# Performance work log

Hardware: AMD Instinct MI355X
Metric: run time of the kernel (lower is better)

The kernel has to match this reference:

```python
import jax, jax.numpy as jnp
import numpy as np

DIM = 128      # token feature dim
HEADS = 4
HEAD_DIM = DIM // HEADS
H = 512
W = 512
NSP = 4096     # n_spixels = H*W/scale
TEMP = DIM ** (-0.5)   # NOTE: original scales by full-dim ** -0.5
NEG = -9.0e15
EPS = 1e-12    # torch F.normalize eps


def setup_inputs() -> dict:
    key = jax.random.key(0)
    k1, k2, k3, k4 = jax.random.split(key, 4)
    return {
        "spf": jax.random.normal(k1, (DIM, NSP), jnp.float32),
        "segments": jax.random.randint(k2, (H, W), 0, NSP, jnp.int32),
        "w_qkv": jax.random.normal(k3, (DIM, 3 * DIM), jnp.float32) / np.sqrt(DIM),
        "w_out": jax.random.normal(k4, (DIM, DIM), jnp.float32) / np.sqrt(DIM),
        "b_out": jnp.zeros((DIM,), jnp.float32),
    }


def build_adjacency(seg, n_sp):
    """Vectorized version of get_A: for every 2x2 window (i in [0,h-3], j in [0,w-3])
    connect the max and min superpixel labels; zero the diagonal."""
    a = seg[:-2, :-2]
    b = seg[:-2, 1:-1]
    c = seg[1:-1, :-2]
    d = seg[1:-1, 1:-1]
    mx = jnp.maximum(jnp.maximum(a, b), jnp.maximum(c, d)).ravel()
    mn = jnp.minimum(jnp.minimum(a, b), jnp.minimum(c, d)).ravel()
    A = jnp.zeros((n_sp, n_sp), jnp.float32)
    A = A.at[mx, mn].set(1.0)
    A = A.at[mn, mx].set(1.0)
    # fill_diagonal(A, 0) (also removes windows where max == min)
    A = A * (1.0 - jnp.eye(n_sp, dtype=jnp.float32))
    return A


def _l2norm(t):
    n = jnp.sqrt(jnp.sum(t * t, axis=-1, keepdims=True))
    return t / jnp.maximum(n, EPS)


def reference(spf, segments, w_qkv, w_out, b_out):
    A = build_adjacency(segments, NSP)                      # [n, n]
    x = spf.T                                               # [n, dim]
    qkv = x @ w_qkv                                         # [n, 3*dim]
    q, k, v = jnp.split(qkv, 3, axis=-1)
    split = lambda t: t.reshape(NSP, HEADS, HEAD_DIM).transpose(1, 0, 2)  # [h, n, d]
    q, k, v = split(q), split(k), split(v)
    q = _l2norm(q)
    k = _l2norm(k)
    # Original masks per-head scores, then keeps only head 0's attention
    # (attn[0][0]) and broadcasts it over all heads' v. We compute only
    # head 0's scores (mathematically identical output).
    scores = (q[0] @ k[0].T) * TEMP                         # [n, n] cosine scores
    scores = jnp.where(A > 0, scores, NEG)
    eye = jnp.eye(NSP, dtype=bool)
    scores = jnp.where(eye, 1.0, scores)                    # np.fill_diagonal(attn, 1)
    attn = jax.nn.softmax(scores, axis=-1)                  # [n, n]
    out = jnp.einsum('nm,hmd->hnd', attn, v)                # shared attn over heads
    out = out.transpose(1, 0, 2).reshape(NSP, DIM)          # [n, dim]
    out = out @ w_out + b_out                               # to_out Linear
    # map_sp2p: scatter superpixel features back to pixel grid (hard assignment)
    pix = out[segments]                                     # [H, W, dim]
    return pix.transpose(2, 0, 1)[None]                     # [1, dim, H, W]
```

## Files before the change

### kernel.cpp

```cpp
#include <hip/hip_runtime.h>

#define NSP 4096
#define HW 512
#define TEMP 0.08838834764831845f
#define MAXE 768

__global__ void zero_mask(unsigned int* __restrict__ mask) {
    int i = blockIdx.x * blockDim.x + threadIdx.x;
    ((uint4*)mask)[i] = make_uint4(0u, 0u, 0u, 0u);
}

__global__ void build_adj(const int* __restrict__ seg, unsigned int* __restrict__ mask) {
    int idx = blockIdx.x * blockDim.x + threadIdx.x;
    const int NW = 510 * 510;
    if (idx >= NW) return;
    int i = idx / 510, j = idx - i * 510;
    const int* r = seg + i * HW + j;
    int a = r[0], b = r[1], c = r[HW], d = r[HW + 1];
    int mx = max(max(a, b), max(c, d));
    int mn = min(min(a, b), min(c, d));
    if (mx == mn) return;
    atomicOr(&mask[mx * 128 + (mn >> 5)], 1u << (mn & 31));
    atomicOr(&mask[mn * 128 + (mx >> 5)], 1u << (mx & 31));
}

__global__ void qkv_gemm(const float* __restrict__ spf, const float* __restrict__ wqkv,
                         float* __restrict__ Q0, float* __restrict__ K0,
                         float* __restrict__ V) {
    int gid = blockIdx.x * blockDim.x + threadIdx.x;
    int g = gid % 48;
    int n = gid / 48;
    int wcol;
    float* outp;
    if (g < 8)       { wcol = g * 4;              outp = Q0 + n * 32  + g * 4; }
    else if (g < 16) { wcol = 128 + (g - 8) * 4;  outp = K0 + n * 32  + (g - 8) * 4; }
    else             { wcol = 256 + (g - 16) * 4; outp = V  + n * 128 + (g - 16) * 4; }
    float4 acc = {0.f, 0.f, 0.f, 0.f};
#pragma unroll 8
    for (int d = 0; d < 128; ++d) {
        float x = spf[d * NSP + n];
        float4 w = *(const float4*)(wqkv + d * 384 + wcol);
        acc.x += x * w.x; acc.y += x * w.y; acc.z += x * w.z; acc.w += x * w.w;
    }
    *(float4*)outp = acc;
}

__global__ void l2norm_qk(float* __restrict__ Q0, float* __restrict__ K0) {
    int t = blockIdx.x * blockDim.x + threadIdx.x;
    float* p = (t < NSP) ? (Q0 + t * 32) : (K0 + (t - NSP) * 32);
    float4* p4 = (float4*)p;
    float4 v[8];
    float s = 0.f;
#pragma unroll
    for (int i = 0; i < 8; ++i) {
        v[i] = p4[i];
        s += v[i].x * v[i].x + v[i].y * v[i].y + v[i].z * v[i].z + v[i].w * v[i].w;
    }
    float inv = 1.0f / fmaxf(sqrtf(s), 1e-12f);
#pragma unroll
    for (int i = 0; i < 8; ++i) {
        v[i].x *= inv; v[i].y *= inv; v[i].z *= inv; v[i].w *= inv;
        p4[i] = v[i];
    }
}

__global__ void __launch_bounds__(128) sparse_attn(
    const unsigned int* __restrict__ mask, const float* __restrict__ Q0,
    const float* __restrict__ K0, const float* __restrict__ V,
    float* __restrict__ out) {
    int n = blockIdx.x;
    int t = threadIdx.x;
    __shared__ int   midx[MAXE];
    __shared__ float wts[MAXE];
    __shared__ int   cnt;
    __shared__ float q0s[32];
    if (t == 0) cnt = 0;
    if (t < 32) q0s[t] = Q0[n * 32 + t];
    __syncthreads();

    unsigned int w = mask[n * 128 + t];
    while (w) {
        int b = __ffs(w) - 1;
        w &= w - 1;
        int m = t * 32 + b;
        const float4* kp = (const float4*)(K0 + m * 32);
        float s = 0.f;
#pragma unroll
        for (int i = 0; i < 8; ++i) {
            float4 kv = kp[i];
            s += q0s[i * 4 + 0] * kv.x + q0s[i * 4 + 1] * kv.y +
                 q0s[i * 4 + 2] * kv.z + q0s[i * 4 + 3] * kv.w;
        }
        float wt = __expf(s * TEMP - 1.0f);
        int pos = atomicAdd(&cnt, 1);
        if (pos < MAXE) { midx[pos] = m; wts[pos] = wt; }
    }
    __syncthreads();

    int c = min(cnt, MAXE);
    float acc  = V[n * 128 + t];
    float wsum = 1.0f;
    int e = 0;
    for (; e + 4 <= c; e += 4) {
        float w0 = wts[e],  w1 = wts[e + 1], w2 = wts[e + 2], w3 = wts[e + 3];
        int   m0 = midx[e], m1 = midx[e + 1], m2 = midx[e + 2], m3 = midx[e + 3];
        float v0 = V[m0 * 128 + t];
        float v1 = V[m1 * 128 + t];
        float v2 = V[m2 * 128 + t];
        float v3 = V[m3 * 128 + t];
        acc  += w0 * v0 + w1 * v1 + w2 * v2 + w3 * v3;
        wsum += w0 + w1 + w2 + w3;
    }
    for (; e < c; ++e) {
        float wt = wts[e];
        acc  += wt * V[midx[e] * 128 + t];
        wsum += wt;
    }
    out[n * 128 + t] = acc / wsum;
}

__global__ void out_gemm(const float* __restrict__ ain, const float* __restrict__ wout,
                         const float* __restrict__ bout, float* __restrict__ final) {
    int gid = blockIdx.x * blockDim.x + threadIdx.x;
    int g = gid & 31;
    int n = gid >> 5;
    const float* arow = ain + n * 128;
    float4 acc = {0.f, 0.f, 0.f, 0.f};
#pragma unroll 8
    for (int d = 0; d < 128; ++d) {
        float a = arow[d];
        float4 w = *(const float4*)(wout + d * 128 + g * 4);
        acc.x += a * w.x; acc.y += a * w.y; acc.z += a * w.z; acc.w += a * w.w;
    }
    float4 b = *(const float4*)(bout + g * 4);
    acc.x += b.x; acc.y += b.y; acc.z += b.z; acc.w += b.w;
    *(float4*)(final + n * 128 + g * 4) = acc;
}

#define GT_PIX 64
__global__ void __launch_bounds__(256) gather_out(
    const float* __restrict__ final, const int* __restrict__ seg,
    float* __restrict__ out) {
    __shared__ float tile[GT_PIX][129];
    __shared__ int   sseg[GT_PIX];
    int base = blockIdx.x * GT_PIX;
    int t = threadIdx.x;
    if (t < GT_PIX) sseg[t] = seg[base + t];
    __syncthreads();

    int c  = t & 127;
    int pl = t >> 7;
#pragma unroll 8
    for (int p = pl; p < GT_PIX; p += 2)
        tile[p][c] = final[sseg[p] * 128 + c];
    __syncthreads();

    int j  = t & 63;
    int c0 = t >> 6;
#pragma unroll 8
    for (int cc = c0; cc < 128; cc += 4)
        out[cc * (HW * HW) + base + j] = tile[j][cc];
}

extern "C" void kernel_launch(void* const* d_in, const int* in_sizes, int n_in,
                              void* d_out, int out_size, void* d_ws, size_t ws_size,
                              hipStream_t stream) {
    const float* spf  = (const float*)d_in[0];
    const int*   seg  = (const int*)d_in[1];
    const float* wqkv = (const float*)d_in[2];
    const float* wout = (const float*)d_in[3];
    const float* bout = (const float*)d_in[4];
    float* out = (float*)d_out;

    char* ws = (char*)d_ws;
    unsigned int* mask = (unsigned int*)ws;
    float* Q0    = (float*)(ws + (2u << 20));
    float* K0    = (float*)(ws + (2u << 20) + (512u << 10));
    float* V     = (float*)(ws + (3u << 20));
    float* aout  = (float*)(ws + (5u << 20));
    float* final = (float*)(ws + (7u << 20));

    hipLaunchKernelGGL(zero_mask,  dim3(512),  dim3(256), 0, stream, mask);
    hipLaunchKernelGGL(build_adj,  dim3((510 * 510 + 255) / 256), dim3(256), 0, stream, seg, mask);
    hipLaunchKernelGGL(qkv_gemm,   dim3(768),  dim3(256), 0, stream, spf, wqkv, Q0, K0, V);
    hipLaunchKernelGGL(l2norm_qk,  dim3(32),   dim3(256), 0, stream, Q0, K0);
    hipLaunchKernelGGL(sparse_attn, dim3(4096), dim3(128), 0, stream, mask, Q0, K0, V, aout);
    hipLaunchKernelGGL(out_gemm,   dim3(512),  dim3(256), 0, stream, aout, wout, bout, final);
    hipLaunchKernelGGL(gather_out, dim3((HW * HW) / GT_PIX), dim3(256), 0, stream, final, seg, out);
}
```

Measured before the change: 241.6 us.

## Fuse adjacency build with QKV GEMM, fold L2 norm, rework attention and gather

The adjacency build and the QKV GEMM now run as one launch with disjoint block ranges, and the Q/K L2 normalization is folded into the GEMM epilogue through lane shuffles. Mask zeroing moves to hipMemsetAsync. In sparse attention, the serial per-word bit loop with a shared atomic counter is replaced by a prefix-sum compaction that spreads edges evenly across threads, and V is gathered as float4 with a reduction across four edge groups. The gather kernel uses float4 loads and stores to cut memory instruction count. In exchange, the attention kernel gains several barriers in the scan and does a binary search plus a bit-clearing loop per edge.

```diff
diff --git a/kernel.cpp b/kernel.cpp
--- a/kernel.cpp
+++ b/kernel.cpp
@@ -4,30 +4,28 @@
 #define HW 512
 #define TEMP 0.08838834764831845f
 #define MAXE 768
-
-__global__ void zero_mask(unsigned int* __restrict__ mask) {
-    int i = blockIdx.x * blockDim.x + threadIdx.x;
-    ((uint4*)mask)[i] = make_uint4(0u, 0u, 0u, 0u);
-}
-
-__global__ void build_adj(const int* __restrict__ seg, unsigned int* __restrict__ mask) {
-    int idx = blockIdx.x * blockDim.x + threadIdx.x;
-    const int NW = 510 * 510;
-    if (idx >= NW) return;
-    int i = idx / 510, j = idx - i * 510;
-    const int* r = seg + i * HW + j;
-    int a = r[0], b = r[1], c = r[HW], d = r[HW + 1];
-    int mx = max(max(a, b), max(c, d));
-    int mn = min(min(a, b), min(c, d));
-    if (mx == mn) return;
-    atomicOr(&mask[mx * 128 + (mn >> 5)], 1u << (mn & 31));
-    atomicOr(&mask[mn * 128 + (mx >> 5)], 1u << (mx & 31));
-}
-
-__global__ void qkv_gemm(const float* __restrict__ spf, const float* __restrict__ wqkv,
-                         float* __restrict__ Q0, float* __restrict__ K0,
-                         float* __restrict__ V) {
-    int gid = blockIdx.x * blockDim.x + threadIdx.x;
+#define ADJ_BLOCKS 1017
+#define QKV_BLOCKS 768
+
+__global__ void __launch_bounds__(256) adj_qkv(
+    const int* __restrict__ seg, unsigned int* __restrict__ mask,
+    const float* __restrict__ spf, const float* __restrict__ wqkv,
+    float* __restrict__ Q0, float* __restrict__ K0, float* __restrict__ V) {
+    int t = threadIdx.x;
+    if (blockIdx.x < ADJ_BLOCKS) {
+        int idx = blockIdx.x * 256 + t;
+        if (idx >= 510 * 510) return;
+        int i = idx / 510, j = idx - i * 510;
+        const int* r = seg + i * HW + j;
+        int a = r[0], b = r[1], c = r[HW], d = r[HW + 1];
+        int mx = max(max(a, b), max(c, d));
+        int mn = min(min(a, b), min(c, d));
+        if (mx == mn) return;
+        atomicOr(&mask[mx * 128 + (mn >> 5)], 1u << (mn & 31));
+        atomicOr(&mask[mn * 128 + (mx >> 5)], 1u << (mx & 31));
+        return;
+    }
+    int gid = (blockIdx.x - ADJ_BLOCKS) * 256 + t;
     int g = gid % 48;
     int n = gid / 48;
     int wcol;
@@ -42,26 +40,15 @@
         float4 w = *(const float4*)(wqkv + d * 384 + wcol);
         acc.x += x * w.x; acc.y += x * w.y; acc.z += x * w.z; acc.w += x * w.w;
     }
+    if (g < 16) {
+        float s = acc.x * acc.x + acc.y * acc.y + acc.z * acc.z + acc.w * acc.w;
+        s += __shfl_xor(s, 1);
+        s += __shfl_xor(s, 2);
+        s += __shfl_xor(s, 4);
+        float inv = 1.0f / fmaxf(sqrtf(s), 1e-12f);
+        acc.x *= inv; acc.y *= inv; acc.z *= inv; acc.w *= inv;
+    }
     *(float4*)outp = acc;
-}
-
-__global__ void l2norm_qk(float* __restrict__ Q0, float* __restrict__ K0) {
-    int t = blockIdx.x * blockDim.x + threadIdx.x;
-    float* p = (t < NSP) ? (Q0 + t * 32) : (K0 + (t - NSP) * 32);
-    float4* p4 = (float4*)p;
-    float4 v[8];
-    float s = 0.f;
-#pragma unroll
-    for (int i = 0; i < 8; ++i) {
-        v[i] = p4[i];
-        s += v[i].x * v[i].x + v[i].y * v[i].y + v[i].z * v[i].z + v[i].w * v[i].w;
-    }
-    float inv = 1.0f / fmaxf(sqrtf(s), 1e-12f);
-#pragma unroll
-    for (int i = 0; i < 8; ++i) {
-        v[i].x *= inv; v[i].y *= inv; v[i].z *= inv; v[i].w *= inv;
-        p4[i] = v[i];
-    }
 }
 
 __global__ void __launch_bounds__(128) sparse_attn(
@@ -70,19 +57,37 @@
     float* __restrict__ out) {
     int n = blockIdx.x;
     int t = threadIdx.x;
+    __shared__ unsigned int words[128];
+    __shared__ int   pfx[128];
     __shared__ int   midx[MAXE];
     __shared__ float wts[MAXE];
-    __shared__ int   cnt;
     __shared__ float q0s[32];
-    if (t == 0) cnt = 0;
+    __shared__ float4 redv[4][32];
+    __shared__ float  redw[4];
+
+    unsigned int w = mask[n * 128 + t];
+    words[t] = w;
     if (t < 32) q0s[t] = Q0[n * 32 + t];
-    __syncthreads();
-
-    unsigned int w = mask[n * 128 + t];
-    while (w) {
-        int b = __ffs(w) - 1;
-        w &= w - 1;
-        int m = t * 32 + b;
+    pfx[t] = __popc(w);
+    __syncthreads();
+#pragma unroll
+    for (int off = 1; off < 128; off <<= 1) {
+        int v = pfx[t];
+        int add = (t >= off) ? pfx[t - off] : 0;
+        __syncthreads();
+        pfx[t] = v + add;
+        __syncthreads();
+    }
+    int E = min(pfx[127], MAXE);
+
+    for (int e = t; e < E; e += 128) {
+        int lo = 0, hi = 127;
+        while (lo < hi) { int mid = (lo + hi) >> 1; if (pfx[mid] > e) hi = mid; else lo = mid + 1; }
+        int base = (lo > 0) ? pfx[lo - 1] : 0;
+        int r = e - base;
+        unsigned int x = words[lo];
+        for (int i = 0; i < r; ++i) x &= x - 1;
+        int m = lo * 32 + (__ffs(x) - 1);
         const float4* kp = (const float4*)(K0 + m * 32);
         float s = 0.f;
 #pragma unroll
@@ -91,32 +96,36 @@
             s += q0s[i * 4 + 0] * kv.x + q0s[i * 4 + 1] * kv.y +
                  q0s[i * 4 + 2] * kv.z + q0s[i * 4 + 3] * kv.w;
         }
-        float wt = __expf(s * TEMP - 1.0f);
-        int pos = atomicAdd(&cnt, 1);
-        if (pos < MAXE) { midx[pos] = m; wts[pos] = wt; }
-    }
-    __syncthreads();
-
-    int c = min(cnt, MAXE);
-    float acc  = V[n * 128 + t];
-    float wsum = 1.0f;
-    int e = 0;
-    for (; e + 4 <= c; e += 4) {
-        float w0 = wts[e],  w1 = wts[e + 1], w2 = wts[e + 2], w3 = wts[e + 3];
-        int   m0 = midx[e], m1 = midx[e + 1], m2 = midx[e + 2], m3 = midx[e + 3];
-        float v0 = V[m0 * 128 + t];
-        float v1 = V[m1 * 128 + t];
-        float v2 = V[m2 * 128 + t];
-        float v3 = V[m3 * 128 + t];
-        acc  += w0 * v0 + w1 * v1 + w2 * v2 + w3 * v3;
-        wsum += w0 + w1 + w2 + w3;
-    }
-    for (; e < c; ++e) {
+        wts[e]  = __expf(s * TEMP - 1.0f);
+        midx[e] = m;
+    }
+    __syncthreads();
+
+    int cg = t & 31, eg = t >> 5;
+    const float4* V4 = (const float4*)V;
+    float4 acc = {0.f, 0.f, 0.f, 0.f};
+    float wp = 0.f;
+    for (int e = eg; e < E; e += 4) {
         float wt = wts[e];
-        acc  += wt * V[midx[e] * 128 + t];
-        wsum += wt;
-    }
-    out[n * 128 + t] = acc / wsum;
+        float4 v = V4[midx[e] * 32 + cg];
+        acc.x += wt * v.x; acc.y += wt * v.y; acc.z += wt * v.z; acc.w += wt * v.w;
+        wp += wt;
+    }
+    redv[eg][cg] = acc;
+    if (cg == 0) redw[eg] = wp;
+    __syncthreads();
+    if (t < 32) {
+        float4 a0 = redv[0][t], a1 = redv[1][t], a2 = redv[2][t], a3 = redv[3][t];
+        float ws = 1.0f + redw[0] + redw[1] + redw[2] + redw[3];
+        float4 vd = V4[n * 32 + t];
+        float inv = 1.0f / ws;
+        float4 o;
+        o.x = (a0.x + a1.x + a2.x + a3.x + vd.x) * inv;
+        o.y = (a0.y + a1.y + a2.y + a3.y + vd.y) * inv;
+        o.z = (a0.z + a1.z + a2.z + a3.z + vd.z) * inv;
+        o.w = (a0.w + a1.w + a2.w + a3.w + vd.w) * inv;
+        ((float4*)out)[n * 32 + t] = o;
+    }
 }
 
 __global__ void out_gemm(const float* __restrict__ ain, const float* __restrict__ wout,
@@ -141,25 +150,35 @@
 __global__ void __launch_bounds__(256) gather_out(
     const float* __restrict__ final, const int* __restrict__ seg,
     float* __restrict__ out) {
-    __shared__ float tile[GT_PIX][129];
-    __shared__ int   sseg[GT_PIX];
+    __shared__ __align__(16) float tile[GT_PIX][132];
+    __shared__ int sseg[GT_PIX];
     int base = blockIdx.x * GT_PIX;
     int t = threadIdx.x;
     if (t < GT_PIX) sseg[t] = seg[base + t];
     __syncthreads();
 
-    int c  = t & 127;
-    int pl = t >> 7;
-#pragma unroll 8
-    for (int p = pl; p < GT_PIX; p += 2)
-        tile[p][c] = final[sseg[p] * 128 + c];
-    __syncthreads();
-
-    int j  = t & 63;
-    int c0 = t >> 6;
-#pragma unroll 8
-    for (int cc = c0; cc < 128; cc += 4)
-        out[cc * (HW * HW) + base + j] = tile[j][cc];
+    int c4 = t & 31, pp = t >> 5;
+    const float4* f4 = (const float4*)final;
+#pragma unroll
+    for (int i = 0; i < 8; ++i) {
+        int p = pp + 8 * i;
+        float4 v = f4[sseg[p] * 32 + c4];
+        *(float4*)&tile[p][c4 * 4] = v;
+    }
+    __syncthreads();
+
+    int jp = t >> 4;
+    int cg = t & 15;
+#pragma unroll
+    for (int pass = 0; pass < 8; ++pass) {
+        int cc = cg + 16 * pass;
+        float4 v;
+        v.x = tile[4 * jp + 0][cc];
+        v.y = tile[4 * jp + 1][cc];
+        v.z = tile[4 * jp + 2][cc];
+        v.w = tile[4 * jp + 3][cc];
+        *(float4*)(out + (size_t)cc * (HW * HW) + base + 4 * jp) = v;
+    }
 }
 
 extern "C" void kernel_launch(void* const* d_in, const int* in_sizes, int n_in,
@@ -180,10 +199,9 @@
     float* aout  = (float*)(ws + (5u << 20));
     float* final = (float*)(ws + (7u << 20));
 
-    hipLaunchKernelGGL(zero_mask,  dim3(512),  dim3(256), 0, stream, mask);
-    hipLaunchKernelGGL(build_adj,  dim3((510 * 510 + 255) / 256), dim3(256), 0, stream, seg, mask);
-    hipLaunchKernelGGL(qkv_gemm,   dim3(768),  dim3(256), 0, stream, spf, wqkv, Q0, K0, V);
-    hipLaunchKernelGGL(l2norm_qk,  dim3(32),   dim3(256), 0, stream, Q0, K0);
+    hipMemsetAsync(mask, 0, NSP * 128 * sizeof(unsigned int), stream);
+    hipLaunchKernelGGL(adj_qkv, dim3(ADJ_BLOCKS + QKV_BLOCKS), dim3(256), 0, stream,
+                       seg, mask, spf, wqkv, Q0, K0, V);
     hipLaunchKernelGGL(sparse_attn, dim3(4096), dim3(128), 0, stream, mask, Q0, K0, V, aout);
     hipLaunchKernelGGL(out_gemm,   dim3(512),  dim3(256), 0, stream, aout, wout, bout, final);
     hipLaunchKernelGGL(gather_out, dim3((HW * HW) / GT_PIX), dim3(256), 0, stream, final, seg, out);
```

Measured after the change: 221.4 us. -8.3%, faster.
